# Kernel tuning notes

Measured on AMD Instinct MI355X. Metric: run time of the kernel, lower is better.

The kernel has to match this reference:

```python
import jax, jax.numpy as jnp
import numpy as np

B, C, N, K, R, PART = 2, 64, 16384, 16, 16, 6
_reps = [C // PART] * (PART - 1) + [C - (C // PART) * (PART - 1)]
_RIDX = np.repeat(np.arange(PART), _reps)  # torch.repeat_interleave index map (6 -> C)


def setup_inputs() -> dict:
    key = jax.random.key(0)
    ks = jax.random.split(key, 26)
    f = lambda i, sh: jax.random.normal(ks[i], sh, jnp.float32)
    u = lambda i, sh: jax.random.uniform(ks[i], sh, jnp.float32, 0.5, 1.5)
    return {
        'x': f(0, (B, C, N)),
        'xyz': f(1, (B, 3, N)) * 0.5,
        'idx': jax.random.randint(ks[2], (B, N, K), 0, N),
        'w3a': f(3, (C, 1, 3, 3, 3)) * 0.1, 'b3a': f(4, (C,)) * 0.1,
        'g3a': u(5, (C,)), 'be3a': f(6, (C,)) * 0.1, 'm3a': f(7, (C,)) * 0.1, 'v3a': u(8, (C,)),
        'w3b': f(9, (C, 1, 3, 3, 3)) * 0.1, 'b3b': f(10, (C,)) * 0.1,
        'g3b': u(11, (C,)), 'be3b': f(12, (C,)) * 0.1, 'm3b': f(13, (C,)) * 0.1, 'v3b': u(14, (C,)),
        'wp1': f(15, (3, C)) * 0.1, 'gp': u(16, (3,)), 'bp': f(17, (3,)) * 0.1,
        'mp': f(18, (3,)) * 0.1, 'vp': u(19, (3,)),
        'wp2': f(20, (3, 3)) * 0.3,
        'gt': u(21, (C,)), 'bt': f(22, (C,)) * 0.1, 'mt': f(23, (C,)) * 0.1, 'vt': u(24, (C,)),
    }


def _bn(x, g, b, m, v, eps):
    sh = (1, -1) + (1,) * (x.ndim - 2)
    return (x - m.reshape(sh)) * (g.reshape(sh) * jax.lax.rsqrt(v.reshape(sh) + eps)) + b.reshape(sh)


def _lrelu(x):
    return jnp.where(x > 0, x, 0.1 * x)


def _forward(x, xyz, idx, w3a, b3a, g3a, be3a, m3a, v3a, w3b, b3b, g3b, be3b, m3b, v3b,
             wp1, gp, bp, mp, vp, wp2, gt, bt, mt, vt):
    # --- voxelization: scatter-average points into R^3 grid (PVCNN, normalize=False) ---
    nc = jnp.clip((xyz - xyz.mean(axis=2, keepdims=True) + 1.0) * 0.5 * R, 0.0, R - 1.0)  # [B,3,N]
    vi = jnp.round(nc).astype(jnp.int32)
    flat = (vi[:, 0] * R + vi[:, 1]) * R + vi[:, 2]  # [B,N]
    seg = lambda fe, s: jax.ops.segment_sum(fe, s, num_segments=R ** 3)
    sums = jax.vmap(lambda xb, sb: seg(xb.T, sb))(x, flat)                    # [B,R^3,C]
    cnts = jax.vmap(lambda sb: seg(jnp.ones((N,), x.dtype), sb))(flat)        # [B,R^3]
    grid = (sums / jnp.maximum(cnts, 1.0)[..., None]).transpose(0, 2, 1).reshape(B, C, R, R, R)
    # --- depthwise 3x3x3 conv3d -> BN3d(eps=1e-4) -> LeakyReLU(0.1), twice ---
    dn = ('NCDHW', 'OIDHW', 'NCDHW')
    h = jax.lax.conv_general_dilated(grid, w3a, (1, 1, 1), 'SAME', dimension_numbers=dn,
                                     feature_group_count=C) + b3a.reshape(1, C, 1, 1, 1)
    h = _lrelu(_bn(h, g3a, be3a, m3a, v3a, 1e-4))
    h = jax.lax.conv_general_dilated(h, w3b, (1, 1, 1), 'SAME', dimension_numbers=dn,
                                     feature_group_count=C) + b3b.reshape(1, C, 1, 1, 1)
    h = _lrelu(_bn(h, g3b, be3b, m3b, v3b, 1e-4))
    # --- trilinear devoxelize: gather 8 corners with trilinear weights ---
    gridf = h.reshape(B, C, R * R * R)
    c0 = jnp.floor(nc).astype(jnp.int32)
    c1 = jnp.minimum(c0 + 1, R - 1)
    fr = nc - c0.astype(nc.dtype)
    p_v_x = jnp.zeros((B, C, N), x.dtype)
    for dx in (0, 1):
        for dy in (0, 1):
            for dz in (0, 1):
                ix = c1[:, 0] if dx else c0[:, 0]
                iy = c1[:, 1] if dy else c0[:, 1]
                iz = c1[:, 2] if dz else c0[:, 2]
                w = ((fr[:, 0] if dx else 1 - fr[:, 0]) *
                     (fr[:, 1] if dy else 1 - fr[:, 1]) *
                     (fr[:, 2] if dz else 1 - fr[:, 2]))  # [B,N]
                fi = (ix * R + iy) * R + iz
                p_v_x = p_v_x + jnp.take_along_axis(gridf, fi[:, None, :], axis=2) * w[:, None, :]
    # --- point branch: gather K neighbors by precomputed ball-query idx ---
    x_j = jnp.take_along_axis(x[:, :, None, :], idx[:, None, :, :], axis=3)      # [B,C,N,K]
    xyz_j = jnp.take_along_axis(xyz[:, :, None, :], idx[:, None, :, :], axis=3)  # [B,3,N,K]
    dp1 = xyz_j - xyz[:, :, :, None]                                             # [B,3,N,K]
    df = x_j - x[:, :, :, None]                                                  # [B,C,N,K]
    # proj_conv: 1x1 conv C->3, BN2d(eps=1e-5), ReLU, 1x1 conv 3->3
    t = jax.nn.relu(_bn(jnp.einsum('oc,bcnk->bonk', wp1, df), gp, bp, mp, vp, 1e-5))
    dp2 = jnp.einsum('op,bpnk->bonk', wp2, t)
    dp = jnp.concatenate([dp1, dp2], axis=1)   # [B,6,N,K]
    wgt = dp[:, _RIDX]                         # repeat_interleave(6 -> C)
    x_j = jax.nn.relu(_bn(x_j * wgt, gt, bt, mt, vt, 1e-5))  # proj_transform
    p_p_x = jnp.max(x_j, axis=-1)              # max-pool over neighbors
    return p_v_x + p_p_x                       # agg_way == 'add'


def reference(x, xyz, idx, w3a, b3a, g3a, be3a, m3a, v3a, w3b, b3b, g3b, be3b, m3b, v3b,
              wp1, gp, bp, mp, vp, wp2, gt, bt, mt, vt):
    return _forward(x, xyz, idx, w3a, b3a, g3a, be3a, m3a, v3a, w3b, b3b, g3b, be3b, m3b, v3b,
                    wp1, gp, bp, mp, vp, wp2, gt, bt, mt, vt)
```

## Files before the change

### kernel.cpp

```cpp
#include <hip/hip_runtime.h>
#include <math.h>

#define BB 2
#define CC 64
#define NPTS 16384
#define KK 16
#define RR 16
#define R3 4096

__device__ __forceinline__ unsigned short f2b(float f) {
  unsigned int u = __float_as_uint(f);
  unsigned int r = u + 0x7fffu + ((u >> 16) & 1u);
  return (unsigned short)(r >> 16);
}
__device__ __forceinline__ float b2f(unsigned short h) {
  return __uint_as_float(((unsigned int)h) << 16);
}

__global__ __launch_bounds__(256) void k_zero_mean(const float* __restrict__ xyz,
                                                   float* __restrict__ meanv,
                                                   float4* __restrict__ zbase,
                                                   int zcount4) {
  int gt = blockIdx.x * 256 + threadIdx.x;
  int stride = gridDim.x * 256;
  for (int i = gt; i < zcount4; i += stride)
    zbase[i] = make_float4(0.f, 0.f, 0.f, 0.f);

  if (blockIdx.x < 6) {
    int row = blockIdx.x;
    const float* src = xyz + (size_t)row * NPTS;
    float s = 0.f;
    for (int i = threadIdx.x; i < NPTS; i += 256) s += src[i];
    for (int off = 32; off; off >>= 1) s += __shfl_down(s, off, 64);
    __shared__ float ls[4];
    int lane = threadIdx.x & 63, wv = threadIdx.x >> 6;
    if (lane == 0) ls[wv] = s;
    __syncthreads();
    if (threadIdx.x == 0) meanv[row] = (ls[0] + ls[1] + ls[2] + ls[3]) / (float)NPTS;
  }
}

__global__ __launch_bounds__(256) void k_prep(
    const float* __restrict__ x, const float* __restrict__ xyz,
    const float* __restrict__ meanv, const float* __restrict__ wp1,
    float* __restrict__ sumsVC, float* __restrict__ cnts,
    unsigned short* __restrict__ xTb, float* __restrict__ rec,
    float* __restrict__ ncT) {
  __shared__ float tile[64][65];
  __shared__ int lflat[64];
  int bi = blockIdx.x;
  int b = bi >> 8, n0 = (bi & 255) * 64;
  int t = threadIdx.x;

  if (t < 64) {
    int n = n0 + t;
    int p = b * NPTS + n;
    float vv[3]; int vi[3];
#pragma unroll
    for (int o = 0; o < 3; ++o) {
      float v = xyz[((size_t)b * 3 + o) * NPTS + n];
      float tc = (v - meanv[b * 3 + o] + 1.0f) * 0.5f * (float)RR;
      tc = fminf(fmaxf(tc, 0.f), (float)(RR - 1));
      vv[o] = tc;
      vi[o] = (int)rintf(tc);
      rec[(size_t)p * 8 + o] = v;
    }
    int f = (vi[0] * RR + vi[1]) * RR + vi[2];
    lflat[t] = f;
    atomicAdd(&cnts[b * R3 + f], 1.0f);
    ((float4*)ncT)[p] = make_float4(vv[0], vv[1], vv[2], 0.f);
  }

  int nl = t & 63, cq = t >> 6;
#pragma unroll 4
  for (int it = 0; it < 16; ++it) {
    int c = it * 4 + cq;
    tile[c][nl] = x[((size_t)b * CC + c) * NPTS + n0 + nl];
  }
  __syncthreads();
  int cw = t & 63, nq = t >> 6;
#pragma unroll 4
  for (int it = 0; it < 16; ++it) {
    int n2 = it * 4 + nq;
    xTb[((size_t)(b * NPTS + n0 + n2)) * 64 + cw] = f2b(tile[cw][n2]);
  }
  int wv = t >> 6, lane = t & 63;
#pragma unroll 2
  for (int i = 0; i < 16; ++i) {
    int n2 = wv * 16 + i;
    atomicAdd(&sumsVC[((size_t)b * R3 + lflat[n2]) * 64 + lane], tile[lane][n2]);
  }
  if (t < 192) {
    int pt = t & 63, o = t >> 6;
    const float* wr = wp1 + o * 64;
    float s = 0.f;
#pragma unroll 8
    for (int c = 0; c < 64; ++c) s += wr[c] * tile[c][pt];
    rec[((size_t)(b * NPTS + n0 + pt)) * 8 + 3 + o] = s;
  }
}

__global__ __launch_bounds__(256) void k_conv(
    const float* __restrict__ sumsVC, const float* __restrict__ cnts,
    const float* __restrict__ w3a, const float* __restrict__ b3a,
    const float* __restrict__ g3a, const float* __restrict__ be3a,
    const float* __restrict__ m3a, const float* __restrict__ v3a,
    const float* __restrict__ w3b, const float* __restrict__ b3b,
    const float* __restrict__ g3b, const float* __restrict__ be3b,
    const float* __restrict__ m3b, const float* __restrict__ v3b,
    unsigned short* __restrict__ gridb) {
  __shared__ float A[12 * 256];
  __shared__ float Ba[10 * 256];
  int bi = blockIdx.x;
  int b = bi >> 7, rem = bi & 127, c = rem >> 1, half = rem & 1;
  int d0 = half * 8;
  int t = threadIdx.x;

  const float* cp = cnts + (size_t)b * R3;
#pragma unroll
  for (int it = 0; it < 12; ++it) {
    int i = t + it * 256;
    int s = it, hw = t;
    int da = d0 - 2 + s;
    float val = 0.f;
    if ((unsigned)da < 16u) {
      int v = (da << 8) + hw;
      val = sumsVC[((size_t)b * R3 + v) * 64 + c] / fmaxf(cp[v], 1.0f);
    }
    A[i] = val;
  }
  float wk[27];
#pragma unroll
  for (int i = 0; i < 27; ++i) wk[i] = w3a[c * 27 + i];
  float bias = b3a[c];
  float sc = g3a[c] * rsqrtf(v3a[c] + 1e-4f);
  float mn = m3a[c], bt2 = be3a[c];
  __syncthreads();
#pragma unroll
  for (int it = 0; it < 10; ++it) {
    int s = it;
    int da = d0 - 1 + s;
    int h = t >> 4, w = t & 15;
    float out = 0.f;
    if ((unsigned)da < 16u) {
      float acc = 0.f;
#pragma unroll
      for (int kd = 0; kd < 3; ++kd) {
        const float* Asl = &A[(s + kd) * 256];
#pragma unroll
        for (int kh = 0; kh < 3; ++kh) {
          int hh = h + kh - 1;
          if ((unsigned)hh < 16u) {
#pragma unroll
            for (int kw = 0; kw < 3; ++kw) {
              int ww = w + kw - 1;
              if ((unsigned)ww < 16u)
                acc += wk[kd * 9 + kh * 3 + kw] * Asl[(hh << 4) + ww];
            }
          }
        }
      }
      acc += bias;
      acc = (acc - mn) * sc + bt2;
      out = acc > 0.f ? acc : 0.1f * acc;
    }
    Ba[s * 256 + t] = out;
  }
#pragma unroll
  for (int i = 0; i < 27; ++i) wk[i] = w3b[c * 27 + i];
  bias = b3b[c];
  sc = g3b[c] * rsqrtf(v3b[c] + 1e-4f);
  mn = m3b[c]; bt2 = be3b[c];
  __syncthreads();
#pragma unroll
  for (int it = 0; it < 8; ++it) {
    int s = it;
    int db = d0 + s;
    int h = t >> 4, w = t & 15;
    float acc = 0.f;
#pragma unroll
    for (int kd = 0; kd < 3; ++kd) {
      const float* Bsl = &Ba[(s + kd) * 256];
#pragma unroll
      for (int kh = 0; kh < 3; ++kh) {
        int hh = h + kh - 1;
        if ((unsigned)hh < 16u) {
#pragma unroll
          for (int kw = 0; kw < 3; ++kw) {
            int ww = w + kw - 1;
            if ((unsigned)ww < 16u)
              acc += wk[kd * 9 + kh * 3 + kw] * Bsl[(hh << 4) + ww];
          }
        }
      }
    }
    acc += bias;
    acc = (acc - mn) * sc + bt2;
    acc = acc > 0.f ? acc : 0.1f * acc;
    gridb[((size_t)b * R3 + (db << 8) + t) * 64 + c] = f2b(acc);
  }
}

__global__ __launch_bounds__(256) void k_final(
    const unsigned short* __restrict__ xTb, const float* __restrict__ rec,
    const float* __restrict__ ncT, const unsigned short* __restrict__ gridb,
    const int* __restrict__ idx,
    const float* __restrict__ gp, const float* __restrict__ bp,
    const float* __restrict__ mp, const float* __restrict__ vp,
    const float* __restrict__ wp2,
    const float* __restrict__ gt, const float* __restrict__ bt,
    const float* __restrict__ mt, const float* __restrict__ vt,
    float* __restrict__ out) {
  __shared__ float wgt[32 * 16 * 7];
  __shared__ float res[64][33];
  int t = threadIdx.x;
  int g = blockIdx.x;
  int b = (g & 7) >> 2;
  int w = ((g >> 3) << 2) + (g & 3);
  int n0 = w * 32;
  int p0 = b * NPTS + n0;
  int bBase = b * NPTS;
  const float4* rec4 = (const float4*)rec;

  {
    float sp0 = gp[0] * rsqrtf(vp[0] + 1e-5f);
    float sp1 = gp[1] * rsqrtf(vp[1] + 1e-5f);
    float sp2 = gp[2] * rsqrtf(vp[2] + 1e-5f);
    float mp0 = mp[0], mp1 = mp[1], mp2 = mp[2];
    float bp0 = bp[0], bp1 = bp[1], bp2 = bp[2];
#pragma unroll
    for (int it = 0; it < 2; ++it) {
      int pair = t + it * 256;
      int pl = pair >> 4, k = pair & 15;
      int p = p0 + pl;
      int j = idx[(size_t)p * 16 + k];
      float4 r0 = rec4[(size_t)p * 2], r1 = rec4[(size_t)p * 2 + 1];
      int pj = bBase + j;
      float4 q0 = rec4[(size_t)pj * 2], q1 = rec4[(size_t)pj * 2 + 1];
      float d0 = q0.x - r0.x, d1 = q0.y - r0.y, d2 = q0.z - r0.z;
      float e0 = q0.w - r0.w, e1 = q1.x - r1.x, e2 = q1.y - r1.y;
      float t0 = fmaxf((e0 - mp0) * sp0 + bp0, 0.f);
      float t1 = fmaxf((e1 - mp1) * sp1 + bp1, 0.f);
      float t2 = fmaxf((e2 - mp2) * sp2 + bp2, 0.f);
      float* wp = &wgt[pair * 7];
      wp[0] = d0; wp[1] = d1; wp[2] = d2;
      wp[3] = wp2[0] * t0 + wp2[1] * t1 + wp2[2] * t2;
      wp[4] = wp2[3] * t0 + wp2[4] * t1 + wp2[5] * t2;
      wp[5] = wp2[6] * t0 + wp2[7] * t1 + wp2[8] * t2;
      ((int*)wp)[6] = j;
    }
  }
  __syncthreads();

  int c = t & 63, wv = t >> 6;
  float st = gt[c] * rsqrtf(vt[c] + 1e-5f);
  float mtc = mt[c], btc = bt[c];
  int part = c / 10; if (part > 5) part = 5;
  const float4* nc4 = (const float4*)ncT;
  const unsigned short* gbase = gridb + (size_t)b * R3 * 64;

#pragma unroll
  for (int pi = 0; pi < 8; ++pi) {
    int pl = wv * 8 + pi;
    int p = p0 + pl;
    float4 ncv = nc4[p];
    float c0x = floorf(ncv.x), c0y = floorf(ncv.y), c0z = floorf(ncv.z);
    int i0x = (int)c0x, i0y = (int)c0y, i0z = (int)c0z;
    int i1x = min(i0x + 1, 15), i1y = min(i0y + 1, 15), i1z = min(i0z + 1, 15);
    float fx = ncv.x - c0x, fy = ncv.y - c0y, fz = ncv.z - c0z;
    float pv = 0.f;
#pragma unroll
    for (int dx = 0; dx < 2; ++dx)
#pragma unroll
      for (int dy = 0; dy < 2; ++dy)
#pragma unroll
        for (int dz = 0; dz < 2; ++dz) {
          int ix = dx ? i1x : i0x, iy = dy ? i1y : i0y, iz = dz ? i1z : i0z;
          float wg = (dx ? fx : 1.f - fx) * (dy ? fy : 1.f - fy) * (dz ? fz : 1.f - fz);
          pv += wg * b2f(gbase[(size_t)((ix * 16 + iy) * 16 + iz) * 64 + c]);
        }
    const float* wrow = &wgt[pl * 16 * 7];
    int jv[16];
#pragma unroll
    for (int k = 0; k < 16; ++k) jv[k] = ((const int*)wrow)[k * 7 + 6];
    unsigned short xv[16];
#pragma unroll
    for (int k = 0; k < 16; ++k) xv[k] = xTb[((size_t)(bBase + jv[k])) * 64 + c];
    float a = -1e30f;
#pragma unroll
    for (int k = 0; k < 16; ++k) {
      float w2 = wrow[k * 7 + part];
      float v = fmaxf((b2f(xv[k]) * w2 - mtc) * st + btc, 0.f);
      a = fmaxf(a, v);
    }
    res[c][pl] = pv + a;
  }
  __syncthreads();
  int col = t & 31, rq = t >> 5;
#pragma unroll
  for (int r = 0; r < 8; ++r) {
    int row = rq + r * 8;
    out[((size_t)(b * CC + row)) * NPTS + n0 + col] = res[row][col];
  }
}

extern "C" void kernel_launch(void* const* d_in, const int* in_sizes, int n_in,
                              void* d_out, int out_size, void* d_ws, size_t ws_size,
                              hipStream_t stream) {
  const float* x    = (const float*)d_in[0];
  const float* xyz  = (const float*)d_in[1];
  const int*   idx  = (const int*)d_in[2];
  const float* w3a  = (const float*)d_in[3];
  const float* b3a  = (const float*)d_in[4];
  const float* g3a  = (const float*)d_in[5];
  const float* be3a = (const float*)d_in[6];
  const float* m3a  = (const float*)d_in[7];
  const float* v3a  = (const float*)d_in[8];
  const float* w3b  = (const float*)d_in[9];
  const float* b3b  = (const float*)d_in[10];
  const float* g3b  = (const float*)d_in[11];
  const float* be3b = (const float*)d_in[12];
  const float* m3b  = (const float*)d_in[13];
  const float* v3b  = (const float*)d_in[14];
  const float* wp1  = (const float*)d_in[15];
  const float* gp   = (const float*)d_in[16];
  const float* bp   = (const float*)d_in[17];
  const float* mp   = (const float*)d_in[18];
  const float* vp   = (const float*)d_in[19];
  const float* wp2  = (const float*)d_in[20];
  const float* gt   = (const float*)d_in[21];
  const float* bt   = (const float*)d_in[22];
  const float* mt   = (const float*)d_in[23];
  const float* vt   = (const float*)d_in[24];

  float* ws     = (float*)d_ws;
  float* sumsVC = ws;
  float* cnts   = sumsVC + 524288;
  float* meanv  = cnts + 8192;
  float* ncT    = meanv + 8;
  float* rec    = ncT + 131072;
  unsigned short* xTb   = (unsigned short*)(rec + 262144);
  unsigned short* gridb = xTb + 2097152;

  k_zero_mean<<<128, 256, 0, stream>>>(xyz, meanv, (float4*)sumsVC, 133120);
  k_prep<<<512, 256, 0, stream>>>(x, xyz, meanv, wp1, sumsVC, cnts, xTb, rec, ncT);
  k_conv<<<256, 256, 0, stream>>>(sumsVC, cnts, w3a, b3a, g3a, be3a, m3a, v3a,
                                  w3b, b3b, g3b, be3b, m3b, v3b, gridb);
  k_final<<<1024, 256, 0, stream>>>(xTb, rec, ncT, gridb, idx,
                                    gp, bp, mp, vp, wp2,
                                    gt, bt, mt, vt, (float*)d_out);
}
```

Baseline: 79.59 us.

## Split fused depthwise conv3d into two channel-coalesced kernels with bf16 intermediate

Replaces the single fused conv kernel, which runs 256 blocks and stages per-channel depth slabs in shared memory, with two kernels of 2048 blocks each. In the new kernels each thread computes one voxel-channel output and reads neighbours straight from global memory in channel-contiguous layout. The first conv's output goes through a bf16 global buffer. The aim is more parallelism and coalesced access in place of strided per-channel gathers, at the cost of an extra launch, extra global traffic from 27 neighbour reads per output, and bf16 rounding of the intermediate.

```diff
diff --git a/kernel.cpp b/kernel.cpp
--- a/kernel.cpp
+++ b/kernel.cpp
@@ -100,105 +100,94 @@
   }
 }
 
-__global__ __launch_bounds__(256) void k_conv(
+__global__ __launch_bounds__(256) void k_conv_a(
     const float* __restrict__ sumsVC, const float* __restrict__ cnts,
     const float* __restrict__ w3a, const float* __restrict__ b3a,
     const float* __restrict__ g3a, const float* __restrict__ be3a,
     const float* __restrict__ m3a, const float* __restrict__ v3a,
+    unsigned short* __restrict__ gA) {
+  int bid = blockIdx.x;
+  int b = (bid & 7) >> 2;
+  int inner = ((bid >> 3) << 2) + (bid & 3);
+  int t = threadIdx.x;
+  int c = t & 63, vq = t >> 6;
+  int v = inner * 4 + vq;
+  int d = v >> 8, h = (v >> 4) & 15, w = v & 15;
+  const float* sp = sumsVC + (size_t)b * R3 * 64;
+  const float* cp = cnts + (size_t)b * R3;
+  float wk[27];
+#pragma unroll
+  for (int i = 0; i < 27; ++i) wk[i] = w3a[c * 27 + i];
+  float acc = 0.f;
+#pragma unroll
+  for (int kd = 0; kd < 3; ++kd) {
+    int dd = d + kd - 1;
+    if ((unsigned)dd < 16u) {
+#pragma unroll
+      for (int kh = 0; kh < 3; ++kh) {
+        int hh = h + kh - 1;
+        if ((unsigned)hh < 16u) {
+#pragma unroll
+          for (int kw = 0; kw < 3; ++kw) {
+            int ww = w + kw - 1;
+            if ((unsigned)ww < 16u) {
+              int nv = (dd << 8) + (hh << 4) + ww;
+              float rc = __builtin_amdgcn_rcpf(fmaxf(cp[nv], 1.f));
+              acc += wk[kd * 9 + kh * 3 + kw] * (sp[(size_t)nv * 64 + c] * rc);
+            }
+          }
+        }
+      }
+    }
+  }
+  acc += b3a[c];
+  acc = (acc - m3a[c]) * (g3a[c] * rsqrtf(v3a[c] + 1e-4f)) + be3a[c];
+  acc = acc > 0.f ? acc : 0.1f * acc;
+  gA[((size_t)b * R3 + v) * 64 + c] = f2b(acc);
+}
+
+__global__ __launch_bounds__(256) void k_conv_b(
+    const unsigned short* __restrict__ gA,
     const float* __restrict__ w3b, const float* __restrict__ b3b,
     const float* __restrict__ g3b, const float* __restrict__ be3b,
     const float* __restrict__ m3b, const float* __restrict__ v3b,
     unsigned short* __restrict__ gridb) {
-  __shared__ float A[12 * 256];
-  __shared__ float Ba[10 * 256];
-  int bi = blockIdx.x;
-  int b = bi >> 7, rem = bi & 127, c = rem >> 1, half = rem & 1;
-  int d0 = half * 8;
+  int bid = blockIdx.x;
+  int b = (bid & 7) >> 2;
+  int inner = ((bid >> 3) << 2) + (bid & 3);
   int t = threadIdx.x;
-
-  const float* cp = cnts + (size_t)b * R3;
-#pragma unroll
-  for (int it = 0; it < 12; ++it) {
-    int i = t + it * 256;
-    int s = it, hw = t;
-    int da = d0 - 2 + s;
-    float val = 0.f;
-    if ((unsigned)da < 16u) {
-      int v = (da << 8) + hw;
-      val = sumsVC[((size_t)b * R3 + v) * 64 + c] / fmaxf(cp[v], 1.0f);
-    }
-    A[i] = val;
-  }
+  int c = t & 63, vq = t >> 6;
+  int v = inner * 4 + vq;
+  int d = v >> 8, h = (v >> 4) & 15, w = v & 15;
+  const unsigned short* sp = gA + (size_t)b * R3 * 64;
   float wk[27];
 #pragma unroll
-  for (int i = 0; i < 27; ++i) wk[i] = w3a[c * 27 + i];
-  float bias = b3a[c];
-  float sc = g3a[c] * rsqrtf(v3a[c] + 1e-4f);
-  float mn = m3a[c], bt2 = be3a[c];
-  __syncthreads();
-#pragma unroll
-  for (int it = 0; it < 10; ++it) {
-    int s = it;
-    int da = d0 - 1 + s;
-    int h = t >> 4, w = t & 15;
-    float out = 0.f;
-    if ((unsigned)da < 16u) {
-      float acc = 0.f;
-#pragma unroll
-      for (int kd = 0; kd < 3; ++kd) {
-        const float* Asl = &A[(s + kd) * 256];
-#pragma unroll
-        for (int kh = 0; kh < 3; ++kh) {
-          int hh = h + kh - 1;
-          if ((unsigned)hh < 16u) {
-#pragma unroll
-            for (int kw = 0; kw < 3; ++kw) {
-              int ww = w + kw - 1;
-              if ((unsigned)ww < 16u)
-                acc += wk[kd * 9 + kh * 3 + kw] * Asl[(hh << 4) + ww];
+  for (int i = 0; i < 27; ++i) wk[i] = w3b[c * 27 + i];
+  float acc = 0.f;
+#pragma unroll
+  for (int kd = 0; kd < 3; ++kd) {
+    int dd = d + kd - 1;
+    if ((unsigned)dd < 16u) {
+#pragma unroll
+      for (int kh = 0; kh < 3; ++kh) {
+        int hh = h + kh - 1;
+        if ((unsigned)hh < 16u) {
+#pragma unroll
+          for (int kw = 0; kw < 3; ++kw) {
+            int ww = w + kw - 1;
+            if ((unsigned)ww < 16u) {
+              int nv = (dd << 8) + (hh << 4) + ww;
+              acc += wk[kd * 9 + kh * 3 + kw] * b2f(sp[(size_t)nv * 64 + c]);
             }
           }
         }
       }
-      acc += bias;
-      acc = (acc - mn) * sc + bt2;
-      out = acc > 0.f ? acc : 0.1f * acc;
-    }
-    Ba[s * 256 + t] = out;
-  }
-#pragma unroll
-  for (int i = 0; i < 27; ++i) wk[i] = w3b[c * 27 + i];
-  bias = b3b[c];
-  sc = g3b[c] * rsqrtf(v3b[c] + 1e-4f);
-  mn = m3b[c]; bt2 = be3b[c];
-  __syncthreads();
-#pragma unroll
-  for (int it = 0; it < 8; ++it) {
-    int s = it;
-    int db = d0 + s;
-    int h = t >> 4, w = t & 15;
-    float acc = 0.f;
-#pragma unroll
-    for (int kd = 0; kd < 3; ++kd) {
-      const float* Bsl = &Ba[(s + kd) * 256];
-#pragma unroll
-      for (int kh = 0; kh < 3; ++kh) {
-        int hh = h + kh - 1;
-        if ((unsigned)hh < 16u) {
-#pragma unroll
-          for (int kw = 0; kw < 3; ++kw) {
-            int ww = w + kw - 1;
-            if ((unsigned)ww < 16u)
-              acc += wk[kd * 9 + kh * 3 + kw] * Bsl[(hh << 4) + ww];
-          }
-        }
-      }
-    }
-    acc += bias;
-    acc = (acc - mn) * sc + bt2;
-    acc = acc > 0.f ? acc : 0.1f * acc;
-    gridb[((size_t)b * R3 + (db << 8) + t) * 64 + c] = f2b(acc);
-  }
+    }
+  }
+  acc += b3b[c];
+  acc = (acc - m3b[c]) * (g3b[c] * rsqrtf(v3b[c] + 1e-4f)) + be3b[c];
+  acc = acc > 0.f ? acc : 0.1f * acc;
+  gridb[((size_t)b * R3 + v) * 64 + c] = f2b(acc);
 }
 
 __global__ __launch_bounds__(256) void k_final(
@@ -341,11 +330,12 @@
   float* rec    = ncT + 131072;
   unsigned short* xTb   = (unsigned short*)(rec + 262144);
   unsigned short* gridb = xTb + 2097152;
+  unsigned short* gA    = gridb + 524288;
 
   k_zero_mean<<<128, 256, 0, stream>>>(xyz, meanv, (float4*)sumsVC, 133120);
   k_prep<<<512, 256, 0, stream>>>(x, xyz, meanv, wp1, sumsVC, cnts, xTb, rec, ncT);
-  k_conv<<<256, 256, 0, stream>>>(sumsVC, cnts, w3a, b3a, g3a, be3a, m3a, v3a,
-                                  w3b, b3b, g3b, be3b, m3b, v3b, gridb);
+  k_conv_a<<<2048, 256, 0, stream>>>(sumsVC, cnts, w3a, b3a, g3a, be3a, m3a, v3a, gA);
+  k_conv_b<<<2048, 256, 0, stream>>>(gA, w3b, b3b, g3b, be3b, m3b, v3b, gridb);
   k_final<<<1024, 256, 0, stream>>>(xTb, rec, ncT, gridb, idx,
                                     gp, bp, mp, vp, wp2,
                                     gt, bt, mt, vt, (float*)d_out);
```

Result: faster. 75.05 us (-5.7%).
